# Kernel tuning notes

Measured on AMD Instinct MI355X. Metric: run time of the kernel, lower is better.

## Reference

```python
import jax, jax.numpy as jnp
import numpy as np

# LIF decay constants: alpha = exp(-dt/tau_syn), beta = exp(-dt/tau_mem)
ALPHA = float(np.exp(-0.001 / 0.01))   # ~0.9048
BETA = float(np.exp(-0.001 / 0.005))   # ~0.8187


@jax.custom_vjp
def spike_fn(x):
    # HeavisideSigmoidApprox: Heaviside forward, sigmoid-derivative surrogate backward
    return (x > 0).astype(x.dtype)

def _spike_fwd(x):
    return spike_fn(x), x

def _spike_bwd(x, g):
    s = jax.nn.sigmoid(x)
    return (g * s * (1.0 - s),)

spike_fn.defvjp(_spike_fwd, _spike_bwd)


def lif_layer(spikes_in, W, R):
    """spikes_in: [B,T,F] -> (spikes [B,T,H], potentials [B,T,H])"""
    h = jnp.einsum('btf,fo->bto', spikes_in, W)  # [B,T,H]
    B, T, H = h.shape
    zeros = jnp.zeros((B, H), h.dtype)

    def step(carry, h_t):
        cur, pot, spk = carry
        rec = spk @ R                      # recurrent current from previous spikes
        new_spk = spike_fn(pot - 1.0)      # threshold at 1.0
        active = 1.0 - jax.lax.stop_gradient(new_spk)  # reset: .detach() in torch
        new_cur = ALPHA * cur + h_t + rec
        new_pot = (BETA * pot + new_cur) * active
        return (new_cur, new_pot, new_spk), (new_pot, new_spk)

    _, (pots, spks) = jax.lax.scan(step, (zeros, zeros, zeros), jnp.swapaxes(h, 0, 1))
    return jnp.swapaxes(spks, 0, 1), jnp.swapaxes(pots, 0, 1)


def readout_rnn(spikes, Wout):
    """spikes: [B,T,H] -> output potentials [B,T+1,O] (leading zero record)"""
    h = jnp.einsum('btf,fo->bto', spikes, Wout)  # [B,T,O]
    B, T, O = h.shape
    zeros = jnp.zeros((B, O), h.dtype)

    def step(carry, h_t):
        cur, pot = carry
        cur = ALPHA * cur + h_t
        pot = BETA * pot + cur
        return (cur, pot), pot

    _, pots = jax.lax.scan(step, (zeros, zeros), jnp.swapaxes(h, 0, 1))
    return jnp.concatenate([zeros[:, None, :], jnp.swapaxes(pots, 0, 1)], axis=1)


def _xavier(key, shape):
    std = np.sqrt(2.0 / (shape[0] + shape[1]))
    return jax.random.normal(key, shape, dtype=jnp.float32) * std


def setup_inputs() -> dict:
    key = jax.random.key(0)
    ks = jax.random.split(key, 6)
    B, T, F, H, O = 256, 100, 256, 1024, 8
    return {
        'inputs': jax.random.normal(ks[0], (B, T, F), dtype=jnp.float32),
        'W0': _xavier(ks[1], (F, H)),
        'W1': _xavier(ks[2], (H, H)),
        'R0': _xavier(ks[3], (H, H)),
        'R1': _xavier(ks[4], (H, H)),
        'Wout': _xavier(ks[5], (H, O)),
    }


def reference(inputs, W0, W1, R0, R1, Wout):
    s1, v1 = lif_layer(inputs, W0, R0)
    s2, v2 = lif_layer(s1, W1, R1)
    out = readout_rnn(s2, Wout)  # [B, T+1, O]
    return (out, s1, s2, v1, v2)
```

## Files before the change

kernel.cpp:

```cpp
#include <hip/hip_runtime.h>


#define SNN_B 256
#define SNN_T 100
#define SNN_F 256
#define SNN_H 1024
#define SNN_O 8

#define ALPHA 0.9048374180359595f
#define BETA  0.8187307530779818f

__global__ __launch_bounds__(256) void gemm_f32(
    const float* __restrict__ A, const float* __restrict__ Bm,
    float* __restrict__ C, int M, int N, int K)
{
    __shared__ float As[16][68];
    __shared__ float Bs[16][64];

    const int tid = threadIdx.x;
    const int m0 = blockIdx.y * 64;
    const int n0 = blockIdx.x * 64;
    const int tm = tid >> 4;
    const int tn = tid & 15;

    const int lrowA = tid >> 2;
    const int lkA   = (tid & 3) * 4;
    const int lkB   = tid >> 4;
    const int lnB   = (tid & 15) * 4;

    float acc[4][4] = {};

    for (int k0 = 0; k0 < K; k0 += 16) {
        float4 a = *(const float4*)&A[(size_t)(m0 + lrowA) * K + k0 + lkA];
        As[lkA + 0][lrowA] = a.x;
        As[lkA + 1][lrowA] = a.y;
        As[lkA + 2][lrowA] = a.z;
        As[lkA + 3][lrowA] = a.w;
        *(float4*)&Bs[lkB][lnB] =
            *(const float4*)&Bm[(size_t)(k0 + lkB) * N + n0 + lnB];
        __syncthreads();
        #pragma unroll
        for (int k = 0; k < 16; ++k) {
            float4 av = *(const float4*)&As[k][tm * 4];
            float4 bv = *(const float4*)&Bs[k][tn * 4];
            float am[4] = {av.x, av.y, av.z, av.w};
            float bn[4] = {bv.x, bv.y, bv.z, bv.w};
            #pragma unroll
            for (int i = 0; i < 4; ++i)
                #pragma unroll
                for (int j = 0; j < 4; ++j)
                    acc[i][j] = fmaf(am[i], bn[j], acc[i][j]);
        }
        __syncthreads();
    }

    #pragma unroll
    for (int i = 0; i < 4; ++i) {
        float4 o = make_float4(acc[i][0], acc[i][1], acc[i][2], acc[i][3]);
        *(float4*)&C[(size_t)(m0 + tm * 4 + i) * N + n0 + tn * 4] = o;
    }
}

__global__ __launch_bounds__(256) void lif_scan(
    const float* __restrict__ hbuf,
    const float* __restrict__ R,
    float* __restrict__ s_out,
    float* __restrict__ v_out)
{
    __shared__ __align__(16) int slist[SNN_H];
    __shared__ int wtot[4];
    __shared__ int sn;

    const int tid = threadIdx.x;
    const int b = blockIdx.x;
    const int c4 = tid << 2;
    const int wv = tid >> 6;
    const int lane = tid & 63;
    const float* __restrict__ Rc = R + c4;

    float4 cur = make_float4(0.f, 0.f, 0.f, 0.f);
    float4 pot = make_float4(0.f, 0.f, 0.f, 0.f);

    if (tid == 0) sn = 0;
    __syncthreads();

    const float* hrow = hbuf + (size_t)b * SNN_T * SNN_H + c4;
    float*       srow = s_out + (size_t)b * SNN_T * SNN_H + c4;
    float*       vrow = v_out + (size_t)b * SNN_T * SNN_H + c4;

    for (int t = 0; t < SNN_T; ++t) {
        float4 hv = *(const float4*)hrow;
        hrow += SNN_H;

        const int n = sn;
        float a0 = 0.f, a1 = 0.f, a2 = 0.f, a3 = 0.f;
        int i = 0;
        for (; i + 4 <= n; i += 4) {
            const int4 ks = *(const int4*)&slist[i];
            const float4 r0 = *(const float4*)(Rc + ((size_t)ks.x << 10));
            const float4 r1 = *(const float4*)(Rc + ((size_t)ks.y << 10));
            const float4 r2 = *(const float4*)(Rc + ((size_t)ks.z << 10));
            const float4 r3 = *(const float4*)(Rc + ((size_t)ks.w << 10));
            a0 += r0.x; a0 += r1.x; a0 += r2.x; a0 += r3.x;
            a1 += r0.y; a1 += r1.y; a1 += r2.y; a1 += r3.y;
            a2 += r0.z; a2 += r1.z; a2 += r2.z; a2 += r3.z;
            a3 += r0.w; a3 += r1.w; a3 += r2.w; a3 += r3.w;
        }
        for (; i < n; ++i) {
            const float4 r0 = *(const float4*)(Rc + ((size_t)slist[i] << 10));
            a0 += r0.x; a1 += r0.y; a2 += r0.z; a3 += r0.w;
        }

        const bool p0 = (pot.x - 1.0f) > 0.0f;
        const bool p1 = (pot.y - 1.0f) > 0.0f;
        const bool p2 = (pot.z - 1.0f) > 0.0f;
        const bool p3 = (pot.w - 1.0f) > 0.0f;
        const float s0 = p0 ? 1.0f : 0.0f;
        const float s1v = p1 ? 1.0f : 0.0f;
        const float s2v = p2 ? 1.0f : 0.0f;
        const float s3 = p3 ? 1.0f : 0.0f;

        cur.x = fmaf(ALPHA, cur.x, hv.x) + a0;
        cur.y = fmaf(ALPHA, cur.y, hv.y) + a1;
        cur.z = fmaf(ALPHA, cur.z, hv.z) + a2;
        cur.w = fmaf(ALPHA, cur.w, hv.w) + a3;
        pot.x = fmaf(BETA, pot.x, cur.x) * (1.0f - s0);
        pot.y = fmaf(BETA, pot.y, cur.y) * (1.0f - s1v);
        pot.z = fmaf(BETA, pot.z, cur.z) * (1.0f - s2v);
        pot.w = fmaf(BETA, pot.w, cur.w) * (1.0f - s3);

        *(float4*)srow = make_float4(s0, s1v, s2v, s3);
        *(float4*)vrow = pot;
        srow += SNN_H; vrow += SNN_H;

        const unsigned long long m0 = __ballot(p0);
        const unsigned long long m1 = __ballot(p1);
        const unsigned long long m2 = __ballot(p2);
        const unsigned long long m3 = __ballot(p3);
        const unsigned long long lt = (1ull << lane) - 1ull;
        const int lpre = __popcll(m0 & lt) + __popcll(m1 & lt)
                       + __popcll(m2 & lt) + __popcll(m3 & lt);
        const int wt = __popcll(m0) + __popcll(m1) + __popcll(m2) + __popcll(m3);
        if (lane == 0) wtot[wv] = wt;
        __syncthreads();
        int off = lpre;
        #pragma unroll
        for (int q = 0; q < 3; ++q)
            if (q < wv) off += wtot[q];
        if (p0) slist[off++] = c4 + 0;
        if (p1) slist[off++] = c4 + 1;
        if (p2) slist[off++] = c4 + 2;
        if (p3) slist[off++] = c4 + 3;
        if (tid == 0) sn = wtot[0] + wtot[1] + wtot[2] + wtot[3];
        __syncthreads();
    }
}

__global__ __launch_bounds__(256) void readout_gemm(
    const float* __restrict__ s2in, const float* __restrict__ Wout,
    float* __restrict__ h3)
{
    const int gid = blockIdx.x * 256 + threadIdx.x;
    const int row = gid >> 3;
    const int o = gid & 7;
    const float* srow = s2in + (size_t)row * SNN_H;
    float acc = 0.f;
    for (int k = 0; k < SNN_H; k += 4) {
        float4 s = *(const float4*)&srow[k];
        acc = fmaf(s.x, Wout[(k + 0) * SNN_O + o], acc);
        acc = fmaf(s.y, Wout[(k + 1) * SNN_O + o], acc);
        acc = fmaf(s.z, Wout[(k + 2) * SNN_O + o], acc);
        acc = fmaf(s.w, Wout[(k + 3) * SNN_O + o], acc);
    }
    h3[(size_t)row * SNN_O + o] = acc;
}

__global__ __launch_bounds__(256) void readout_scan(
    const float* __restrict__ h3, float* __restrict__ out)
{
    const int gid = blockIdx.x * 256 + threadIdx.x;
    const int b = gid >> 3;
    const int o = gid & 7;
    float c = 0.f, p = 0.f;
    out[((size_t)b * (SNN_T + 1) + 0) * SNN_O + o] = 0.f;
    for (int t = 0; t < SNN_T; ++t) {
        c = fmaf(ALPHA, c, h3[((size_t)b * SNN_T + t) * SNN_O + o]);
        p = fmaf(BETA, p, c);
        out[((size_t)b * (SNN_T + 1) + t + 1) * SNN_O + o] = p;
    }
}

extern "C" void kernel_launch(void* const* d_in, const int* in_sizes, int n_in,
                              void* d_out, int out_size, void* d_ws, size_t ws_size,
                              hipStream_t stream)
{
    const float* X    = (const float*)d_in[0];
    const float* W0   = (const float*)d_in[1];
    const float* W1   = (const float*)d_in[2];
    const float* R0   = (const float*)d_in[3];
    const float* R1   = (const float*)d_in[4];
    const float* Wout = (const float*)d_in[5];

    const size_t BT_H = (size_t)SNN_B * SNN_T * SNN_H;
    float* out = (float*)d_out;
    float* s1  = out + (size_t)SNN_B * (SNN_T + 1) * SNN_O;
    float* s2  = s1 + BT_H;
    float* v1  = s2 + BT_H;
    float* v2  = v1 + BT_H;

    float* ws   = (float*)d_ws;
    float* hbuf = ws;
    float* h3   = hbuf + BT_H;

    const int M = SNN_B * SNN_T;

    gemm_f32<<<dim3(SNN_H / 64, M / 64), 256, 0, stream>>>(X, W0, hbuf, M, SNN_H, SNN_F);

    lif_scan<<<SNN_B, 256, 0, stream>>>(hbuf, R0, s1, v1);

    gemm_f32<<<dim3(SNN_H / 64, M / 64), 256, 0, stream>>>(s1, W1, hbuf, M, SNN_H, SNN_H);

    lif_scan<<<SNN_B, 256, 0, stream>>>(hbuf, R1, s2, v2);

    readout_gemm<<<(M * SNN_O) / 256, 256, 0, stream>>>(s2, Wout, h3);
    readout_scan<<<(SNN_B * SNN_O) / 256, 256, 0, stream>>>(h3, out);
}
```

Baseline: 3.383 ms.

## Use one thread per neuron in LIF scan with double-buffered sparse row gathers

The LIF scan block grows from 256 to 1024 threads, so each thread owns one hidden neuron instead of four. The sparse recurrent gather is restructured into chunks of 8 spike indices with software double-buffering of the loads, to keep more memory requests in flight. This aims to raise memory-level parallelism and occupancy in the latency-bound scan. In exchange, each gather becomes a scalar 4-byte load instead of a float4, and more waves take part in each per-step barrier.

```diff
diff --git a/kernel.cpp b/kernel.cpp
--- a/kernel.cpp
+++ b/kernel.cpp
@@ -61,97 +61,108 @@
     }
 }
 
-__global__ __launch_bounds__(256) void lif_scan(
+
+#define LIF_LOAD(Xa, Xb, Xc, Xd, Xe, Xf, Xg, Xh, cidx)                        \
+    {                                                                         \
+        const int4 ka_ = *(const int4*)&slist[(cidx) << 3];                   \
+        const int4 kb_ = *(const int4*)&slist[((cidx) << 3) + 4];             \
+        Xa = Rc[(size_t)ka_.x << 10];                                         \
+        Xb = Rc[(size_t)ka_.y << 10];                                         \
+        Xc = Rc[(size_t)ka_.z << 10];                                         \
+        Xd = Rc[(size_t)ka_.w << 10];                                         \
+        Xe = Rc[(size_t)kb_.x << 10];                                         \
+        Xf = Rc[(size_t)kb_.y << 10];                                         \
+        Xg = Rc[(size_t)kb_.z << 10];                                         \
+        Xh = Rc[(size_t)kb_.w << 10];                                         \
+    }
+
+#define LIF_SUM(Xa, Xb, Xc, Xd, Xe, Xf, Xg, Xh)                               \
+    {                                                                         \
+        a0 += Xa; a0 += Xb; a0 += Xc; a0 += Xd;                               \
+        a0 += Xe; a0 += Xf; a0 += Xg; a0 += Xh;                               \
+    }
+
+__global__ __launch_bounds__(1024) void lif_scan(
     const float* __restrict__ hbuf,
     const float* __restrict__ R,
     float* __restrict__ s_out,
     float* __restrict__ v_out)
 {
     __shared__ __align__(16) int slist[SNN_H];
-    __shared__ int wtot[4];
+    __shared__ int wtot[16];
     __shared__ int sn;
 
     const int tid = threadIdx.x;
     const int b = blockIdx.x;
-    const int c4 = tid << 2;
     const int wv = tid >> 6;
     const int lane = tid & 63;
-    const float* __restrict__ Rc = R + c4;
-
-    float4 cur = make_float4(0.f, 0.f, 0.f, 0.f);
-    float4 pot = make_float4(0.f, 0.f, 0.f, 0.f);
+    const float* __restrict__ Rc = R + tid;
+
+    float cur = 0.f, pot = 0.f;
 
     if (tid == 0) sn = 0;
     __syncthreads();
 
-    const float* hrow = hbuf + (size_t)b * SNN_T * SNN_H + c4;
-    float*       srow = s_out + (size_t)b * SNN_T * SNN_H + c4;
-    float*       vrow = v_out + (size_t)b * SNN_T * SNN_H + c4;
+    const float* hrow = hbuf + (size_t)b * SNN_T * SNN_H + tid;
+    float*       srow = s_out + (size_t)b * SNN_T * SNN_H + tid;
+    float*       vrow = v_out + (size_t)b * SNN_T * SNN_H + tid;
 
     for (int t = 0; t < SNN_T; ++t) {
-        float4 hv = *(const float4*)hrow;
+        const float hv = *hrow;
         hrow += SNN_H;
 
         const int n = sn;
-        float a0 = 0.f, a1 = 0.f, a2 = 0.f, a3 = 0.f;
+        float a0 = 0.f;
         int i = 0;
-        for (; i + 4 <= n; i += 4) {
-            const int4 ks = *(const int4*)&slist[i];
-            const float4 r0 = *(const float4*)(Rc + ((size_t)ks.x << 10));
-            const float4 r1 = *(const float4*)(Rc + ((size_t)ks.y << 10));
-            const float4 r2 = *(const float4*)(Rc + ((size_t)ks.z << 10));
-            const float4 r3 = *(const float4*)(Rc + ((size_t)ks.w << 10));
-            a0 += r0.x; a0 += r1.x; a0 += r2.x; a0 += r3.x;
-            a1 += r0.y; a1 += r1.y; a1 += r2.y; a1 += r3.y;
-            a2 += r0.z; a2 += r1.z; a2 += r2.z; a2 += r3.z;
-            a3 += r0.w; a3 += r1.w; a3 += r2.w; a3 += r3.w;
+        const int nc = n >> 3;
+        if (nc > 0) {
+            float A0, A1, A2, A3, A4, A5, A6, A7;
+            float B0, B1, B2, B3, B4, B5, B6, B7;
+            LIF_LOAD(A0, A1, A2, A3, A4, A5, A6, A7, 0);
+            int c = 1;
+            for (; c + 1 < nc; c += 2) {
+                LIF_LOAD(B0, B1, B2, B3, B4, B5, B6, B7, c);
+                LIF_SUM(A0, A1, A2, A3, A4, A5, A6, A7);
+                LIF_LOAD(A0, A1, A2, A3, A4, A5, A6, A7, c + 1);
+                LIF_SUM(B0, B1, B2, B3, B4, B5, B6, B7);
+            }
+            if (c < nc) {
+                LIF_LOAD(B0, B1, B2, B3, B4, B5, B6, B7, c);
+                LIF_SUM(A0, A1, A2, A3, A4, A5, A6, A7);
+                LIF_SUM(B0, B1, B2, B3, B4, B5, B6, B7);
+            } else {
+                LIF_SUM(A0, A1, A2, A3, A4, A5, A6, A7);
+            }
+            i = nc << 3;
         }
-        for (; i < n; ++i) {
-            const float4 r0 = *(const float4*)(Rc + ((size_t)slist[i] << 10));
-            a0 += r0.x; a1 += r0.y; a2 += r0.z; a3 += r0.w;
-        }
-
-        const bool p0 = (pot.x - 1.0f) > 0.0f;
-        const bool p1 = (pot.y - 1.0f) > 0.0f;
-        const bool p2 = (pot.z - 1.0f) > 0.0f;
-        const bool p3 = (pot.w - 1.0f) > 0.0f;
-        const float s0 = p0 ? 1.0f : 0.0f;
-        const float s1v = p1 ? 1.0f : 0.0f;
-        const float s2v = p2 ? 1.0f : 0.0f;
-        const float s3 = p3 ? 1.0f : 0.0f;
-
-        cur.x = fmaf(ALPHA, cur.x, hv.x) + a0;
-        cur.y = fmaf(ALPHA, cur.y, hv.y) + a1;
-        cur.z = fmaf(ALPHA, cur.z, hv.z) + a2;
-        cur.w = fmaf(ALPHA, cur.w, hv.w) + a3;
-        pot.x = fmaf(BETA, pot.x, cur.x) * (1.0f - s0);
-        pot.y = fmaf(BETA, pot.y, cur.y) * (1.0f - s1v);
-        pot.z = fmaf(BETA, pot.z, cur.z) * (1.0f - s2v);
-        pot.w = fmaf(BETA, pot.w, cur.w) * (1.0f - s3);
-
-        *(float4*)srow = make_float4(s0, s1v, s2v, s3);
-        *(float4*)vrow = pot;
+        for (; i < n; ++i)
+            a0 += Rc[(size_t)slist[i] << 10];
+
+        const bool p = (pot - 1.0f) > 0.0f;
+        const float s = p ? 1.0f : 0.0f;
+        cur = fmaf(ALPHA, cur, hv) + a0;
+        pot = fmaf(BETA, pot, cur) * (1.0f - s);
+
+        *srow = s;
+        *vrow = pot;
         srow += SNN_H; vrow += SNN_H;
 
-        const unsigned long long m0 = __ballot(p0);
-        const unsigned long long m1 = __ballot(p1);
-        const unsigned long long m2 = __ballot(p2);
-        const unsigned long long m3 = __ballot(p3);
+        const unsigned long long m = __ballot(p);
         const unsigned long long lt = (1ull << lane) - 1ull;
-        const int lpre = __popcll(m0 & lt) + __popcll(m1 & lt)
-                       + __popcll(m2 & lt) + __popcll(m3 & lt);
-        const int wt = __popcll(m0) + __popcll(m1) + __popcll(m2) + __popcll(m3);
-        if (lane == 0) wtot[wv] = wt;
+        const int lpre = __popcll(m & lt);
+        if (lane == 0) wtot[wv] = __popcll(m);
         __syncthreads();
         int off = lpre;
         #pragma unroll
-        for (int q = 0; q < 3; ++q)
+        for (int q = 0; q < 15; ++q)
             if (q < wv) off += wtot[q];
-        if (p0) slist[off++] = c4 + 0;
-        if (p1) slist[off++] = c4 + 1;
-        if (p2) slist[off++] = c4 + 2;
-        if (p3) slist[off++] = c4 + 3;
-        if (tid == 0) sn = wtot[0] + wtot[1] + wtot[2] + wtot[3];
+        if (p) slist[off] = tid;
+        if (tid == 0) {
+            int stot = 0;
+            #pragma unroll
+            for (int q = 0; q < 16; ++q) stot += wtot[q];
+            sn = stot;
+        }
         __syncthreads();
     }
 }
@@ -216,11 +227,11 @@
 
     gemm_f32<<<dim3(SNN_H / 64, M / 64), 256, 0, stream>>>(X, W0, hbuf, M, SNN_H, SNN_F);
 
-    lif_scan<<<SNN_B, 256, 0, stream>>>(hbuf, R0, s1, v1);
+    lif_scan<<<SNN_B, 1024, 0, stream>>>(hbuf, R0, s1, v1);
 
     gemm_f32<<<dim3(SNN_H / 64, M / 64), 256, 0, stream>>>(s1, W1, hbuf, M, SNN_H, SNN_H);
 
-    lif_scan<<<SNN_B, 256, 0, stream>>>(hbuf, R1, s2, v2);
+    lif_scan<<<SNN_B, 1024, 0, stream>>>(hbuf, R1, s2, v2);
 
     readout_gemm<<<(M * SNN_O) / 256, 256, 0, stream>>>(s2, Wout, h3);
     readout_scan<<<(SNN_B * SNN_O) / 256, 256, 0, stream>>>(h3, out);
```

Measured after the change: 3.172 ms. 1.07x faster.
